# Kernel tuning notes

Measured on AMD Instinct MI355X. Metric: run time of the kernel, lower is better.

Reference implementation:

```python
import jax, jax.numpy as jnp
import numpy as np

B, N, C, H, K = 4, 16384, 256, 8, 64
D = C // H
EPS = 1e-8

def setup_inputs() -> dict:
    key = jax.random.key(0)
    ks = jax.random.split(key, 6)
    scale = 0.02
    return {
        "voxel_features": jax.random.normal(ks[0], (B, N, C), dtype=jnp.float32),
        "cluster_assignments": jax.random.uniform(ks[1], (B, N, K), dtype=jnp.float32),
        "w_qkv": jax.random.normal(ks[2], (C, 3 * C), dtype=jnp.float32) * scale,
        "w_proj": jax.random.normal(ks[3], (C, C), dtype=jnp.float32) * scale,
        "b_proj": jnp.zeros((C,), dtype=jnp.float32),
        "cluster_bias": jax.random.normal(ks[4], (K, K), dtype=jnp.float32) * scale,
    }

def reference(voxel_features, cluster_assignments, w_qkv, w_proj, b_proj, cluster_bias):
    b, n, c = voxel_features.shape
    h, d = H, c // H
    A = cluster_assignments                                  # (B,N,K)
    qkv = (voxel_features @ w_qkv).reshape(b, n, 3, h, d)    # (B,N,3,H,D)
    q = jnp.moveaxis(qkv[:, :, 0], 1, 2)                     # (B,H,N,D)
    k = jnp.moveaxis(qkv[:, :, 1], 1, 2)
    v = jnp.moveaxis(qkv[:, :, 2], 1, 2)
    # cluster mass per (batch, cluster)
    denom = A.sum(axis=1) + EPS                              # (B,K)
    # cluster-pooled K/V: contraction over N (the huge broadcast-sum in torch)
    k_cluster = jnp.einsum('bnk,bhnd->bhkd', A, k) / denom[:, None, :, None]
    v_cluster = jnp.einsum('bnk,bhnd->bhkd', A, v) / denom[:, None, :, None]
    attn = jnp.einsum('bhnd,bhkd->bhnk', q, k_cluster) * (d ** -0.5)
    bias = jnp.einsum('bnk,kl->bnl', A, cluster_bias)        # (B,N,K)
    attn = jax.nn.softmax(attn + bias[:, None, :, :], axis=-1)
    x = jnp.einsum('bhnk,bhkd->bhnd', attn, v_cluster)       # (B,H,N,D)
    x = jnp.moveaxis(x, 1, 2).reshape(b, n, c)               # (B,N,C)
    return x @ w_proj + b_proj
```

## Files before the change

### kernel.cpp

```cpp
#include <hip/hip_runtime.h>

#define NTOK 16384
#define BATCH 4

typedef __attribute__((ext_vector_type(8))) short bf16x8;
typedef __attribute__((ext_vector_type(8))) unsigned short ushort8;
typedef __attribute__((ext_vector_type(4))) float f32x4;

__device__ __forceinline__ unsigned short f2bf(float f) {
  union { float f; unsigned int u; } c; c.f = f;
  unsigned int r = c.u + 0x7fff + ((c.u >> 16) & 1);
  return (unsigned short)(r >> 16);
}

__device__ __forceinline__ float exp2_fast(float x) {
  float r;
  asm("v_exp_f32 %0, %1" : "=v"(r) : "v"(x));
  return r;
}

__global__ __launch_bounds__(256) void convx2(const float* __restrict__ voxel,
                                              const float* __restrict__ A,
                                              unsigned short* __restrict__ xb,
                                              unsigned short* __restrict__ Ab) {
  for (int i = blockIdx.x * 256 + threadIdx.x; i < 2621440; i += gridDim.x * 256) {
    const float* src; unsigned short* dst; int j;
    if (i < 2097152) { j = i; src = voxel; dst = xb; }
    else { j = i - 2097152; src = A; dst = Ab; }
    float4 a = *(const float4*)(src + 8 * (size_t)j);
    float4 b = *(const float4*)(src + 8 * (size_t)j + 4);
    ushort8 o;
    o[0] = f2bf(a.x); o[1] = f2bf(a.y); o[2] = f2bf(a.z); o[3] = f2bf(a.w);
    o[4] = f2bf(b.x); o[5] = f2bf(b.y); o[6] = f2bf(b.z); o[7] = f2bf(b.w);
    *(ushort8*)(dst + 8 * (size_t)j) = o;
  }
}

__global__ __launch_bounds__(256) void convw(const float* __restrict__ w_qkv,
                                             const float* __restrict__ w_proj,
                                             const float* __restrict__ cb,
                                             unsigned short* __restrict__ wqT,
                                             unsigned short* __restrict__ wpT,
                                             unsigned short* __restrict__ cbbT,
                                             float* __restrict__ asum) {
  int n = blockIdx.x, k = threadIdx.x;
  if (n < 256) wqT[n * 256 + k] = f2bf(w_qkv[(size_t)k * 768 + n]);
  else if (n < 512) wpT[(n - 256) * 256 + k] = f2bf(w_proj[(size_t)k * 256 + (n - 256)]);
  else {
    asum[k] = 0.f;
    if (k < 64) {
      for (int j = 0; j < 64; ++j)
        cbbT[k * 64 + j] = f2bf(cb[j * 64 + k] * 1.4426950408889634f);
    }
  }
}

template <int ADD_BIAS, int C_BF16>
__global__ __launch_bounds__(256, 3) void gemm_mfma(const unsigned short* __restrict__ Ab,
                                                    const unsigned short* __restrict__ BT,
                                                    const float* __restrict__ bias,
                                                    void* __restrict__ Cv,
                                                    int N, int K, int lda) {
  __shared__ __align__(16) unsigned short smem[2][128][72];
  const int tid = threadIdx.x;
  int bx, by;
  if ((gridDim.y & 7) == 0) {
    int flat = blockIdx.y * gridDim.x + blockIdx.x;
    int xc = flat & 7, t = flat >> 3;
    int gx = gridDim.x, ypx = gridDim.y >> 3;
    bx = t % gx; by = xc * ypx + t / gx;
  } else { bx = blockIdx.x; by = blockIdx.y; }
  const int bn = bx * 128, bm = by * 128;
  const int lane = tid & 63;
  const int wv = tid >> 6;
  const int wm = wv & 1, wn = wv >> 1;
  const int m16 = lane & 15, quad = lane >> 4;

  const int srow = tid >> 1;
  const int scol = (tid & 1) * 32;

  const unsigned short* ga = Ab + (size_t)(bm + srow) * lda + scol;
  const unsigned short* gb = BT + (size_t)(bn + srow) * K + scol;

  ushort8 ra[2][4], rb[2][4];
#pragma unroll
  for (int kt = 0; kt < 2; ++kt)
#pragma unroll
    for (int i = 0; i < 4; ++i) {
      ra[kt][i] = *(const ushort8*)(ga + kt * 64 + 8 * i);
      rb[kt][i] = *(const ushort8*)(gb + kt * 64 + 8 * i);
    }

  f32x4 acc[4][4];
#pragma unroll
  for (int r = 0; r < 4; ++r)
#pragma unroll
    for (int c = 0; c < 4; ++c) acc[r][c] = (f32x4){0.f, 0.f, 0.f, 0.f};

#pragma unroll
  for (int kt = 0; kt < 4; ++kt) {
    const int sb = kt & 1;
    if (kt > 0) __syncthreads();
#pragma unroll
    for (int i = 0; i < 4; ++i) {
      *(ushort8*)&smem[0][srow][scol + 8 * i] = ra[sb][i];
      *(ushort8*)&smem[1][srow][scol + 8 * i] = rb[sb][i];
    }
    __syncthreads();
    if (kt < 2) {
#pragma unroll
      for (int i = 0; i < 4; ++i) {
        ra[sb][i] = *(const ushort8*)(ga + (kt + 2) * 64 + 8 * i);
        rb[sb][i] = *(const ushort8*)(gb + (kt + 2) * 64 + 8 * i);
      }
    }
#pragma unroll
    for (int ks = 0; ks < 64; ks += 32) {
      bf16x8 af[4], bf[4];
#pragma unroll
      for (int r = 0; r < 4; ++r)
        af[r] = *(const bf16x8*)&smem[0][wm * 64 + r * 16 + m16][ks + quad * 8];
#pragma unroll
      for (int c = 0; c < 4; ++c)
        bf[c] = *(const bf16x8*)&smem[1][wn * 64 + c * 16 + m16][ks + quad * 8];
#pragma unroll
      for (int r = 0; r < 4; ++r)
#pragma unroll
        for (int c = 0; c < 4; ++c)
          acc[r][c] = __builtin_amdgcn_mfma_f32_16x16x32_bf16(af[r], bf[c], acc[r][c], 0, 0, 0);
    }
  }

  float bv[4];
  if (ADD_BIAS) {
#pragma unroll
    for (int c = 0; c < 4; ++c) bv[c] = bias[bn + wn * 64 + c * 16 + m16];
  }
  const int lrD = tid >> 2, cch = (tid & 3) * 32;
  unsigned short* Csh = (unsigned short*)smem;
  float* Csf = (float*)smem;
#pragma unroll
  for (int p = 0; p < 2; ++p) {
    __syncthreads();
    if (wm == p) {
#pragma unroll
      for (int r = 0; r < 4; ++r) {
        int lr0 = r * 16 + quad * 4;
#pragma unroll
        for (int c = 0; c < 4; ++c) {
          int col = wn * 64 + c * 16 + m16;
#pragma unroll
          for (int i = 0; i < 4; ++i) {
            float v = acc[r][c][i] + (ADD_BIAS ? bv[c] : 0.f);
            if (C_BF16) Csh[(lr0 + i) * 136 + col] = f2bf(v);
            else Csf[(lr0 + i) * 132 + col] = v;
          }
        }
      }
    }
    __syncthreads();
    if (C_BF16) {
      unsigned short* gp = (unsigned short*)Cv + (size_t)(bm + p * 64 + lrD) * N + bn + cch;
      const unsigned short* sp = Csh + lrD * 136 + cch;
      ushort8 t0 = *(const ushort8*)(sp + 0);
      ushort8 t1 = *(const ushort8*)(sp + 8);
      ushort8 t2 = *(const ushort8*)(sp + 16);
      ushort8 t3 = *(const ushort8*)(sp + 24);
      *(ushort8*)(gp + 0) = t0;
      *(ushort8*)(gp + 8) = t1;
      *(ushort8*)(gp + 16) = t2;
      *(ushort8*)(gp + 24) = t3;
    } else {
      float* gp = (float*)Cv + (size_t)(bm + p * 64 + lrD) * N + bn + cch;
      const float* sp = Csf + lrD * 132 + cch;
      float4 t[8];
#pragma unroll
      for (int u = 0; u < 8; ++u) t[u] = *(const float4*)(sp + 4 * u);
#pragma unroll
      for (int u = 0; u < 8; ++u) *(float4*)(gp + 4 * u) = t[u];
    }
  }
}

__global__ __launch_bounds__(256) void pool_mfma(const unsigned short* __restrict__ Ab,
                                                 const unsigned short* __restrict__ xb,
                                                 float* __restrict__ part) {
  __shared__ unsigned short At[64][40];
  __shared__ unsigned short Xt[128][40];
  const int tid = threadIdx.x;
  const int tch = blockIdx.x, cblk = blockIdx.y, b = blockIdx.z;
  const int w = tid >> 6, lane = tid & 63;
  const int m16 = lane & 15, quad = lane >> 4;
  const size_t row0 = (size_t)b * NTOK + (size_t)tch * 256;
  const int cb0 = cblk * 128;
  const int tokL = tid & 31, gA = tid >> 5;

  f32x4 acc[4][2];
#pragma unroll
  for (int r = 0; r < 4; ++r)
#pragma unroll
    for (int c = 0; c < 2; ++c) acc[r][c] = (f32x4){0.f, 0.f, 0.f, 0.f};

  ushort8 px[2], pa;
  auto loadG = [&](int t0) {
#pragma unroll
    for (int u = 0; u < 2; ++u) {
      int idx = tid + u * 256;
      int tok = idx & 31, g = idx >> 5;
      px[u] = *(const ushort8*)(xb + (row0 + t0 + tok) * 256 + cb0 + g * 8);
    }
    pa = *(const ushort8*)(Ab + (row0 + t0 + tokL) * 64 + gA * 8);
  };
  loadG(0);

  for (int ks = 0; ks < 8; ++ks) {
    __syncthreads();
#pragma unroll
    for (int u = 0; u < 2; ++u) {
      int idx = tid + u * 256;
      int tok = idx & 31, g = idx >> 5;
#pragma unroll
      for (int i = 0; i < 8; ++i) Xt[g * 8 + i][tok] = (unsigned short)px[u][i];
    }
#pragma unroll
    for (int i = 0; i < 8; ++i) At[gA * 8 + i][tokL] = (unsigned short)pa[i];
    __syncthreads();
    if (ks + 1 < 8) loadG((ks + 1) * 32);
    bf16x8 af[4], bfr[2];
#pragma unroll
    for (int r = 0; r < 4; ++r) af[r] = *(const bf16x8*)&At[r * 16 + m16][quad * 8];
#pragma unroll
    for (int c = 0; c < 2; ++c) bfr[c] = *(const bf16x8*)&Xt[w * 32 + c * 16 + m16][quad * 8];
#pragma unroll
    for (int r = 0; r < 4; ++r)
#pragma unroll
      for (int c = 0; c < 2; ++c)
        acc[r][c] = __builtin_amdgcn_mfma_f32_16x16x32_bf16(af[r], bfr[c], acc[r][c], 0, 0, 0);
  }

  float* pp = part + ((size_t)(b * 64 + tch) * 64) * 256 + cb0;
#pragma unroll
  for (int r = 0; r < 4; ++r)
#pragma unroll
    for (int c = 0; c < 2; ++c)
#pragma unroll
      for (int i = 0; i < 4; ++i) {
        int cl = r * 16 + quad * 4 + i;
        int ch = w * 32 + c * 16 + m16;
        pp[(size_t)cl * 256 + ch] = acc[r][c][i];
      }
}

__global__ __launch_bounds__(256) void pool2kv(const float* __restrict__ part,
                                               const float* __restrict__ asum,
                                               const float* __restrict__ w_qkv,
                                               unsigned short* __restrict__ kcb,
                                               unsigned short* __restrict__ vcbT) {
  __shared__ float px[256];
  const int bc = blockIdx.x;
  const int b = bc >> 6, cl = bc & 63;
  const int c = threadIdx.x;
  const float* pp = part + ((size_t)(b * 64) * 64 + cl) * 256 + c;
  float s = 0.f;
#pragma unroll 4
  for (int t = 0; t < 64; ++t) s += pp[(size_t)t * 16384];
  float denom = asum[b * 64 + cl] + 1e-8f;
  px[c] = s / denom;
  __syncthreads();
  float accK = 0.f, accV = 0.f;
#pragma unroll 8
  for (int k = 0; k < 256; ++k) {
    float x = px[k];
    accK = fmaf(x, w_qkv[(size_t)k * 768 + 256 + c], accK);
    accV = fmaf(x, w_qkv[(size_t)k * 768 + 512 + c], accV);
  }
  int h = c >> 5, d = c & 31;
  kcb[(((size_t)b * 8 + h) * 64 + cl) * 32 + d] =
      f2bf(accK * (0.17677669529663687f * 1.4426950408889634f));
  vcbT[(((size_t)b * 8 + h) * 32 + d) * 64 + cl] = f2bf(accV);
}

__global__ __launch_bounds__(256) void asum_kernel(const float* __restrict__ A,
                                                   float* __restrict__ asum) {
  __shared__ float red[4][64];
  const int ch = blockIdx.x, b = blockIdx.y;
  const int jq = threadIdx.x >> 6, k = threadIdx.x & 63;
  const size_t row0 = (size_t)b * NTOK + (size_t)ch * 256;
  const float* ap = A + (row0 + jq) * 64 + k;
  float s = 0.f;
#pragma unroll 4
  for (int j = 0; j < 64; ++j) s += ap[(size_t)j * 256];
  red[jq][k] = s;
  __syncthreads();
  if (threadIdx.x < 64) {
    float v = red[0][k] + red[1][k] + red[2][k] + red[3][k];
    atomicAdd(&asum[b * 64 + k], v);
  }
}

__global__ __launch_bounds__(256) void attn_mfma(const unsigned short* __restrict__ Ab,
                                                 unsigned short* __restrict__ qb,
                                                 const unsigned short* __restrict__ kcb,
                                                 const unsigned short* __restrict__ vcbT,
                                                 const unsigned short* __restrict__ cbbT) {
  __shared__ __align__(16) unsigned short PA[64 * 72];

  const int tid = threadIdx.x;
  const int nb = blockIdx.x, b = blockIdx.z;
  const int w = tid >> 6, lane = tid & 63;
  const int m16 = lane & 15, quad = lane >> 4;
  const size_t row0 = (size_t)b * NTOK + (size_t)nb * 64;
  const int rA = w * 16 + m16;
  const size_t bh8 = (size_t)b * 8;

  f32x4 bacc[4];
#pragma unroll
  for (int nt = 0; nt < 4; ++nt) bacc[nt] = (f32x4){0.f, 0.f, 0.f, 0.f};
#pragma unroll
  for (int ks = 0; ks < 2; ++ks) {
    bf16x8 aA = *(const bf16x8*)(Ab + (row0 + rA) * 64 + ks * 32 + quad * 8);
#pragma unroll
    for (int nt = 0; nt < 4; ++nt) {
      bf16x8 cbf = *(const bf16x8*)(cbbT + (nt * 16 + m16) * 64 + ks * 32 + quad * 8);
      bacc[nt] = __builtin_amdgcn_mfma_f32_16x16x32_bf16(aA, cbf, bacc[nt], 0, 0, 0);
    }
  }

  for (int h = 0; h < 8; ++h) {
    bf16x8 qf = *(const bf16x8*)(qb + (row0 + rA) * 256 + h * 32 + quad * 8);
    bf16x8 kcf[4];
#pragma unroll
    for (int nt = 0; nt < 4; ++nt)
      kcf[nt] = *(const bf16x8*)(kcb + ((bh8 + h) * 64 + nt * 16 + m16) * 32 + quad * 8);
    bf16x8 vtf[2][2];
#pragma unroll
    for (int nt2 = 0; nt2 < 2; ++nt2)
#pragma unroll
      for (int kc2 = 0; kc2 < 2; ++kc2)
        vtf[nt2][kc2] = *(const bf16x8*)(vcbT + ((bh8 + h) * 32 + nt2 * 16 + m16) * 64 +
                                         kc2 * 32 + quad * 8);

    f32x4 acc[4];
#pragma unroll
    for (int nt = 0; nt < 4; ++nt) {
      acc[nt] = bacc[nt];
      acc[nt] = __builtin_amdgcn_mfma_f32_16x16x32_bf16(qf, kcf[nt], acc[nt], 0, 0, 0);
    }

    f32x4 mxv, sv;
#pragma unroll
    for (int i = 0; i < 4; ++i)
      mxv[i] = fmaxf(fmaxf(acc[0][i], acc[1][i]), fmaxf(acc[2][i], acc[3][i]));
#pragma unroll
    for (int msk = 1; msk < 16; msk <<= 1)
#pragma unroll
      for (int i = 0; i < 4; ++i) mxv[i] = fmaxf(mxv[i], __shfl_xor(mxv[i], msk));
#pragma unroll
    for (int i = 0; i < 4; ++i) sv[i] = 0.f;
#pragma unroll
    for (int nt = 0; nt < 4; ++nt)
#pragma unroll
      for (int i = 0; i < 4; ++i) {
        float e = exp2_fast(acc[nt][i] - mxv[i]);
        acc[nt][i] = e;
        sv[i] += e;
      }
#pragma unroll
    for (int msk = 1; msk < 16; msk <<= 1)
#pragma unroll
      for (int i = 0; i < 4; ++i) sv[i] += __shfl_xor(sv[i], msk);
#pragma unroll
    for (int i = 0; i < 4; ++i) sv[i] = 1.f / sv[i];

#pragma unroll
    for (int nt = 0; nt < 4; ++nt)
#pragma unroll
      for (int i = 0; i < 4; ++i)
        PA[(w * 16 + quad * 4 + i) * 72 + nt * 16 + m16] = f2bf(acc[nt][i] * sv[i]);

    f32x4 acc2[2];
#pragma unroll
    for (int nt2 = 0; nt2 < 2; ++nt2) acc2[nt2] = (f32x4){0.f, 0.f, 0.f, 0.f};
#pragma unroll
    for (int kc2 = 0; kc2 < 2; ++kc2) {
      bf16x8 pf = *(const bf16x8*)&PA[rA * 72 + kc2 * 32 + quad * 8];
#pragma unroll
      for (int nt2 = 0; nt2 < 2; ++nt2)
        acc2[nt2] = __builtin_amdgcn_mfma_f32_16x16x32_bf16(pf, vtf[nt2][kc2], acc2[nt2], 0, 0, 0);
    }

#pragma unroll
    for (int nt2 = 0; nt2 < 2; ++nt2)
#pragma unroll
      for (int i = 0; i < 4; ++i)
        qb[(row0 + w * 16 + quad * 4 + i) * 256 + h * 32 + nt2 * 16 + m16] =
            f2bf(acc2[nt2][i]);
  }
}

extern "C" void kernel_launch(void* const* d_in, const int* in_sizes, int n_in,
                              void* d_out, int out_size, void* d_ws, size_t ws_size,
                              hipStream_t stream) {
  const float* voxel  = (const float*)d_in[0];
  const float* A      = (const float*)d_in[1];
  const float* w_qkv  = (const float*)d_in[2];
  const float* w_proj = (const float*)d_in[3];
  const float* b_proj = (const float*)d_in[4];
  const float* cb     = (const float*)d_in[5];
  float* out = (float*)d_out;
  (void)in_sizes; (void)n_in; (void)out_size; (void)ws_size;

  char* wsb = (char*)d_ws;
  unsigned short* qb       = (unsigned short*)wsb;
  unsigned short* xb       = (unsigned short*)(wsb + 33554432);
  float* part              = (float*)(wsb + 67108864);
  float* asum              = (float*)(wsb + 83886080);
  unsigned short* wqT      = (unsigned short*)(wsb + 84149248);
  unsigned short* wpT      = (unsigned short*)(wsb + 84280320);
  unsigned short* kcb      = (unsigned short*)(wsb + 84411392);
  unsigned short* vcbT     = (unsigned short*)(wsb + 84542464);
  unsigned short* cbbT     = (unsigned short*)(wsb + 84673536);
  unsigned short* Ab = (unsigned short*)d_out;

  convw<<<513, 256, 0, stream>>>(w_qkv, w_proj, cb, wqT, wpT, cbbT, asum);
  convx2<<<2048, 256, 0, stream>>>(voxel, A, xb, Ab);

  gemm_mfma<0, 1><<<dim3(2, 512), 256, 0, stream>>>(xb, wqT, nullptr, qb,
                                                    256, 256, 256);

  asum_kernel<<<dim3(64, BATCH), 256, 0, stream>>>(A, asum);
  pool_mfma<<<dim3(64, 2, BATCH), 256, 0, stream>>>(Ab, xb, part);
  pool2kv<<<256, 256, 0, stream>>>(part, asum, w_qkv, kcb, vcbT);

  attn_mfma<<<dim3(NTOK / 64, 1, BATCH), 256, 0, stream>>>(Ab, qb, kcb, vcbT, cbbT);

  gemm_mfma<1, 0><<<dim3(2, 512), 256, 0, stream>>>(qb, wpT, b_proj, out,
                                                    256, 256, 256);
}
```

Measured before the change: 277.7 us.

## Fold cluster-mass sums into pooling MFMA and split attention over head groups

Result: faster. 271.6 us (-2.2%).

```diff
diff --git a/kernel.cpp b/kernel.cpp
--- a/kernel.cpp
+++ b/kernel.cpp
@@ -41,17 +41,13 @@
                                              const float* __restrict__ cb,
                                              unsigned short* __restrict__ wqT,
                                              unsigned short* __restrict__ wpT,
-                                             unsigned short* __restrict__ cbbT,
-                                             float* __restrict__ asum) {
+                                             unsigned short* __restrict__ cbbT) {
   int n = blockIdx.x, k = threadIdx.x;
   if (n < 256) wqT[n * 256 + k] = f2bf(w_qkv[(size_t)k * 768 + n]);
   else if (n < 512) wpT[(n - 256) * 256 + k] = f2bf(w_proj[(size_t)k * 256 + (n - 256)]);
-  else {
-    asum[k] = 0.f;
-    if (k < 64) {
-      for (int j = 0; j < 64; ++j)
-        cbbT[k * 64 + j] = f2bf(cb[j * 64 + k] * 1.4426950408889634f);
-    }
+  else if (k < 64) {
+    for (int j = 0; j < 64; ++j)
+      cbbT[k * 64 + j] = f2bf(cb[j * 64 + k] * 1.4426950408889634f);
   }
 }
 
@@ -184,7 +180,8 @@
 
 __global__ __launch_bounds__(256) void pool_mfma(const unsigned short* __restrict__ Ab,
                                                  const unsigned short* __restrict__ xb,
-                                                 float* __restrict__ part) {
+                                                 float* __restrict__ part,
+                                                 float* __restrict__ asump) {
   __shared__ unsigned short At[64][40];
   __shared__ unsigned short Xt[128][40];
   const int tid = threadIdx.x;
@@ -200,6 +197,12 @@
   for (int r = 0; r < 4; ++r)
 #pragma unroll
     for (int c = 0; c < 2; ++c) acc[r][c] = (f32x4){0.f, 0.f, 0.f, 0.f};
+  f32x4 acc1[4];
+#pragma unroll
+  for (int r = 0; r < 4; ++r) acc1[r] = (f32x4){0.f, 0.f, 0.f, 0.f};
+  bf16x8 onesv;
+#pragma unroll
+  for (int i = 0; i < 8; ++i) onesv[i] = (short)0x3F80;
 
   ushort8 px[2], pa;
   auto loadG = [&](int t0) {
@@ -236,6 +239,11 @@
 #pragma unroll
       for (int c = 0; c < 2; ++c)
         acc[r][c] = __builtin_amdgcn_mfma_f32_16x16x32_bf16(af[r], bfr[c], acc[r][c], 0, 0, 0);
+    if (cblk == 0) {
+#pragma unroll
+      for (int r = 0; r < 4; ++r)
+        acc1[r] = __builtin_amdgcn_mfma_f32_16x16x32_bf16(af[r], onesv, acc1[r], 0, 0, 0);
+    }
   }
 
   float* pp = part + ((size_t)(b * 64 + tch) * 64) * 256 + cb0;
@@ -249,23 +257,37 @@
         int ch = w * 32 + c * 16 + m16;
         pp[(size_t)cl * 256 + ch] = acc[r][c][i];
       }
+  if (cblk == 0 && tid < 64 && m16 == 0) {
+    float* ap = asump + ((size_t)(b * 64 + tch)) * 64;
+#pragma unroll
+    for (int r = 0; r < 4; ++r)
+#pragma unroll
+      for (int i = 0; i < 4; ++i)
+        ap[r * 16 + quad * 4 + i] = acc1[r][i];
+  }
 }
 
 __global__ __launch_bounds__(256) void pool2kv(const float* __restrict__ part,
-                                               const float* __restrict__ asum,
+                                               const float* __restrict__ asump,
                                                const float* __restrict__ w_qkv,
                                                unsigned short* __restrict__ kcb,
                                                unsigned short* __restrict__ vcbT) {
   __shared__ float px[256];
+  __shared__ float dsh;
   const int bc = blockIdx.x;
   const int b = bc >> 6, cl = bc & 63;
   const int c = threadIdx.x;
+  if (c < 64) {
+    float av = asump[((size_t)(b * 64) + c) * 64 + cl];
+#pragma unroll
+    for (int msk = 1; msk < 64; msk <<= 1) av += __shfl_xor(av, msk);
+    if (c == 0) dsh = av + 1e-8f;
+  }
   const float* pp = part + ((size_t)(b * 64) * 64 + cl) * 256 + c;
   float s = 0.f;
 #pragma unroll 4
   for (int t = 0; t < 64; ++t) s += pp[(size_t)t * 16384];
-  float denom = asum[b * 64 + cl] + 1e-8f;
-  px[c] = s / denom;
+  px[c] = s;
   __syncthreads();
   float accK = 0.f, accV = 0.f;
 #pragma unroll 8
@@ -274,44 +296,31 @@
     accK = fmaf(x, w_qkv[(size_t)k * 768 + 256 + c], accK);
     accV = fmaf(x, w_qkv[(size_t)k * 768 + 512 + c], accV);
   }
+  float inv = 1.f / dsh;
   int h = c >> 5, d = c & 31;
   kcb[(((size_t)b * 8 + h) * 64 + cl) * 32 + d] =
-      f2bf(accK * (0.17677669529663687f * 1.4426950408889634f));
-  vcbT[(((size_t)b * 8 + h) * 32 + d) * 64 + cl] = f2bf(accV);
-}
-
-__global__ __launch_bounds__(256) void asum_kernel(const float* __restrict__ A,
-                                                   float* __restrict__ asum) {
-  __shared__ float red[4][64];
-  const int ch = blockIdx.x, b = blockIdx.y;
-  const int jq = threadIdx.x >> 6, k = threadIdx.x & 63;
-  const size_t row0 = (size_t)b * NTOK + (size_t)ch * 256;
-  const float* ap = A + (row0 + jq) * 64 + k;
-  float s = 0.f;
-#pragma unroll 4
-  for (int j = 0; j < 64; ++j) s += ap[(size_t)j * 256];
-  red[jq][k] = s;
-  __syncthreads();
-  if (threadIdx.x < 64) {
-    float v = red[0][k] + red[1][k] + red[2][k] + red[3][k];
-    atomicAdd(&asum[b * 64 + k], v);
-  }
+      f2bf(accK * inv * (0.17677669529663687f * 1.4426950408889634f));
+  vcbT[(((size_t)b * 8 + h) * 32 + d) * 64 + cl] = f2bf(accV * inv);
 }
 
 __global__ __launch_bounds__(256) void attn_mfma(const unsigned short* __restrict__ Ab,
-                                                 unsigned short* __restrict__ qb,
+                                                 const unsigned short* __restrict__ qb,
+                                                 unsigned short* __restrict__ xout,
                                                  const unsigned short* __restrict__ kcb,
                                                  const unsigned short* __restrict__ vcbT,
                                                  const unsigned short* __restrict__ cbbT) {
   __shared__ __align__(16) unsigned short PA[64 * 72];
+  __shared__ __align__(16) unsigned short XO[64 * 36];
 
   const int tid = threadIdx.x;
-  const int nb = blockIdx.x, b = blockIdx.z;
+  const int nb = blockIdx.x, hq = blockIdx.y, b = blockIdx.z;
+  const int h0 = hq * 4;
   const int w = tid >> 6, lane = tid & 63;
   const int m16 = lane & 15, quad = lane >> 4;
   const size_t row0 = (size_t)b * NTOK + (size_t)nb * 64;
   const int rA = w * 16 + m16;
   const size_t bh8 = (size_t)b * 8;
+  const int l4 = lane >> 2, s3 = lane & 3;
 
   f32x4 bacc[4];
 #pragma unroll
@@ -326,7 +335,9 @@
     }
   }
 
-  for (int h = 0; h < 8; ++h) {
+#pragma unroll
+  for (int hh = 0; hh < 4; ++hh) {
+    const int h = h0 + hh;
     bf16x8 qf = *(const bf16x8*)(qb + (row0 + rA) * 256 + h * 32 + quad * 8);
     bf16x8 kcf[4];
 #pragma unroll
@@ -342,10 +353,8 @@
 
     f32x4 acc[4];
 #pragma unroll
-    for (int nt = 0; nt < 4; ++nt) {
-      acc[nt] = bacc[nt];
-      acc[nt] = __builtin_amdgcn_mfma_f32_16x16x32_bf16(qf, kcf[nt], acc[nt], 0, 0, 0);
-    }
+    for (int nt = 0; nt < 4; ++nt)
+      acc[nt] = __builtin_amdgcn_mfma_f32_16x16x32_bf16(qf, kcf[nt], bacc[nt], 0, 0, 0);
 
     f32x4 mxv, sv;
 #pragma unroll
@@ -366,17 +375,16 @@
         sv[i] += e;
       }
 #pragma unroll
+    for (int nt = 0; nt < 4; ++nt)
+#pragma unroll
+      for (int i = 0; i < 4; ++i)
+        PA[(w * 16 + quad * 4 + i) * 72 + nt * 16 + m16] = f2bf(acc[nt][i]);
+#pragma unroll
     for (int msk = 1; msk < 16; msk <<= 1)
 #pragma unroll
       for (int i = 0; i < 4; ++i) sv[i] += __shfl_xor(sv[i], msk);
 #pragma unroll
     for (int i = 0; i < 4; ++i) sv[i] = 1.f / sv[i];
-
-#pragma unroll
-    for (int nt = 0; nt < 4; ++nt)
-#pragma unroll
-      for (int i = 0; i < 4; ++i)
-        PA[(w * 16 + quad * 4 + i) * 72 + nt * 16 + m16] = f2bf(acc[nt][i] * sv[i]);
 
     f32x4 acc2[2];
 #pragma unroll
@@ -393,8 +401,9 @@
     for (int nt2 = 0; nt2 < 2; ++nt2)
 #pragma unroll
       for (int i = 0; i < 4; ++i)
-        qb[(row0 + w * 16 + quad * 4 + i) * 256 + h * 32 + nt2 * 16 + m16] =
-            f2bf(acc2[nt2][i]);
+        XO[(w * 16 + quad * 4 + i) * 36 + nt2 * 16 + m16] = f2bf(acc2[nt2][i] * sv[i]);
+    ushort8 xv = *(const ushort8*)&XO[(w * 16 + l4) * 36 + s3 * 8];
+    *(ushort8*)(xout + (row0 + w * 16 + l4) * 256 + h * 32 + s3 * 8) = xv;
   }
 }
 
@@ -414,26 +423,25 @@
   unsigned short* qb       = (unsigned short*)wsb;
   unsigned short* xb       = (unsigned short*)(wsb + 33554432);
   float* part              = (float*)(wsb + 67108864);
-  float* asum              = (float*)(wsb + 83886080);
-  unsigned short* wqT      = (unsigned short*)(wsb + 84149248);
-  unsigned short* wpT      = (unsigned short*)(wsb + 84280320);
-  unsigned short* kcb      = (unsigned short*)(wsb + 84411392);
-  unsigned short* vcbT     = (unsigned short*)(wsb + 84542464);
-  unsigned short* cbbT     = (unsigned short*)(wsb + 84673536);
+  float* asump             = (float*)(wsb + 83886080);
+  unsigned short* wqT      = (unsigned short*)(wsb + 83951616);
+  unsigned short* wpT      = (unsigned short*)(wsb + 84082688);
+  unsigned short* kcb      = (unsigned short*)(wsb + 84213760);
+  unsigned short* vcbT     = (unsigned short*)(wsb + 84344832);
+  unsigned short* cbbT     = (unsigned short*)(wsb + 84475904);
   unsigned short* Ab = (unsigned short*)d_out;
 
-  convw<<<513, 256, 0, stream>>>(w_qkv, w_proj, cb, wqT, wpT, cbbT, asum);
+  convw<<<513, 256, 0, stream>>>(w_qkv, w_proj, cb, wqT, wpT, cbbT);
   convx2<<<2048, 256, 0, stream>>>(voxel, A, xb, Ab);
 
   gemm_mfma<0, 1><<<dim3(2, 512), 256, 0, stream>>>(xb, wqT, nullptr, qb,
                                                     256, 256, 256);
 
-  asum_kernel<<<dim3(64, BATCH), 256, 0, stream>>>(A, asum);
-  pool_mfma<<<dim3(64, 2, BATCH), 256, 0, stream>>>(Ab, xb, part);
-  pool2kv<<<256, 256, 0, stream>>>(part, asum, w_qkv, kcb, vcbT);
-
-  attn_mfma<<<dim3(NTOK / 64, 1, BATCH), 256, 0, stream>>>(Ab, qb, kcb, vcbT, cbbT);
-
-  gemm_mfma<1, 0><<<dim3(2, 512), 256, 0, stream>>>(qb, wpT, b_proj, out,
+  pool_mfma<<<dim3(64, 2, BATCH), 256, 0, stream>>>(Ab, xb, part, asump);
+  pool2kv<<<256, 256, 0, stream>>>(part, asump, w_qkv, kcb, vcbT);
+
+  attn_mfma<<<dim3(NTOK / 64, 2, BATCH), 256, 0, stream>>>(Ab, qb, xb, kcb, vcbT, cbbT);
+
+  gemm_mfma<1, 0><<<dim3(2, 512), 256, 0, stream>>>(xb, wpT, b_proj, out,
                                                     256, 256, 256);
 }
```
